# Kernel optimization log

Measured on AMD Instinct MI355X. Metric: run time of the kernel, lower is better.

The kernel has to match this reference:

```python
import jax, jax.numpy as jnp
import numpy as np

N_NODES = 100000
N_EDGES = 1600000
H = 64
N_LAYERS = 3
NUM_APPS = max(1, N_LAYERS - 1)  # forward applies layer once, then while l>1 loop


def setup_inputs() -> dict:
    key = jax.random.key(0)
    k1, k2, k3, k4, k5 = jax.random.split(key, 5)
    features = jax.random.normal(k1, (N_NODES, H), dtype=jnp.float32)
    W = jax.random.normal(k2, (H, H), dtype=jnp.float32) / np.sqrt(H)
    b = jax.random.normal(k3, (H,), dtype=jnp.float32) * 0.01
    src = jax.random.randint(k4, (N_EDGES,), 0, N_NODES, dtype=jnp.int64)
    dst = jax.random.randint(k5, (N_EDGES,), 0, N_NODES, dtype=jnp.int64)
    return {"features": features, "W": W, "b": b, "src": src, "dst": dst}


def reference(features, W, b, src, dst):
    n = features.shape[0]
    ones = jnp.ones(src.shape[0], dtype=features.dtype)
    # DGL GraphConv norm='both': symmetric normalization, degrees clamped >= 1
    deg_out = jax.ops.segment_sum(ones, src, num_segments=n)
    deg_in = jax.ops.segment_sum(ones, dst, num_segments=n)
    inv_sqrt_out = jnp.clip(deg_out, 1.0, None) ** -0.5  # [N]
    inv_sqrt_in = jnp.clip(deg_in, 1.0, None) ** -0.5    # [N]

    h = features
    for _ in range(NUM_APPS):  # shared-weight GraphConv + ReLU, applied n_layers-1 times
        msg = (h * inv_sqrt_out[:, None])[src]                   # [E, H] gather
        agg = jax.ops.segment_sum(msg, dst, num_segments=n)      # [N, H] scatter-add
        h = jax.nn.relu((agg * inv_sqrt_in[:, None]) @ W + b)    # [N, H]
    return h
```

## Files before the change

### kernel.cpp

```cpp
#include <hip/hip_runtime.h>
#include <hip/hip_fp16.h>

#define N_NODES 100000
#define N_EDGES 1600000
#define HDIM 64
#define NPB 512
#define NPB_SHIFT 9
#define NBUCK ((N_NODES + NPB - 1) / NPB)
#define NCHUNK 512
#define CHUNK (N_EDGES / NCHUNK)

__global__ void hist_kernel(const int* __restrict__ src, const int* __restrict__ dst,
                            int* __restrict__ hbD, int* __restrict__ hbS) {
    __shared__ int hD[NBUCK], hS[NBUCK];
    int t = threadIdx.x, blk = blockIdx.x;
    for (int i = t; i < NBUCK; i += 256) { hD[i] = 0; hS[i] = 0; }
    __syncthreads();
    int e0 = blk * CHUNK;
    for (int i = t; i < CHUNK; i += 256) {
        atomicAdd(&hD[dst[e0 + i] >> NPB_SHIFT], 1);
        atomicAdd(&hS[src[e0 + i] >> NPB_SHIFT], 1);
    }
    __syncthreads();
    for (int i = t; i < NBUCK; i += 256) {
        hbD[i * NCHUNK + blk] = hD[i];
        hbS[i * NCHUNK + blk] = hS[i];
    }
}

__global__ void chunk_scan_kernel(const int* __restrict__ hbD, const int* __restrict__ hbS,
                                  int* __restrict__ pbD, int* __restrict__ pbS,
                                  int* __restrict__ totD, int* __restrict__ totS) {
    __shared__ int s[NCHUNK];
    int b = blockIdx.x, t = threadIdx.x;
    int v = hbD[b * NCHUNK + t];
    s[t] = v;
    __syncthreads();
    for (int off = 1; off < NCHUNK; off <<= 1) {
        int x = (t >= off) ? s[t - off] : 0;
        __syncthreads(); s[t] += x; __syncthreads();
    }
    pbD[b * NCHUNK + t] = s[t] - v;
    if (t == NCHUNK - 1) totD[b] = s[t];
    __syncthreads();
    v = hbS[b * NCHUNK + t];
    s[t] = v;
    __syncthreads();
    for (int off = 1; off < NCHUNK; off <<= 1) {
        int x = (t >= off) ? s[t - off] : 0;
        __syncthreads(); s[t] += x; __syncthreads();
    }
    pbS[b * NCHUNK + t] = s[t] - v;
    if (t == NCHUNK - 1) totS[b] = s[t];
}

__global__ void bucket_base_kernel(const int* __restrict__ totD, const int* __restrict__ totS,
                                   int* __restrict__ baseD, int* __restrict__ baseS) {
    __shared__ int s[256];
    int t = threadIdx.x;
    int v = (t < NBUCK) ? totD[t] : 0;
    s[t] = v;
    __syncthreads();
    for (int off = 1; off < 256; off <<= 1) {
        int x = (t >= off) ? s[t - off] : 0;
        __syncthreads(); s[t] += x; __syncthreads();
    }
    if (t < NBUCK) baseD[t] = s[t] - v;
    __syncthreads();
    v = (t < NBUCK) ? totS[t] : 0;
    s[t] = v;
    __syncthreads();
    for (int off = 1; off < 256; off <<= 1) {
        int x = (t >= off) ? s[t - off] : 0;
        __syncthreads(); s[t] += x; __syncthreads();
    }
    if (t < NBUCK) baseS[t] = s[t] - v;
}

__global__ void place_kernel(const int* __restrict__ src, const int* __restrict__ dst,
                             const int* __restrict__ baseD, const int* __restrict__ pbD,
                             const int* __restrict__ baseS, const int* __restrict__ pbS,
                             unsigned int* __restrict__ bufD, unsigned short* __restrict__ bufS) {
    __shared__ int curD[NBUCK], curS[NBUCK];
    int t = threadIdx.x, blk = blockIdx.x;
    for (int i = t; i < NBUCK; i += 256) {
        curD[i] = baseD[i] + pbD[i * NCHUNK + blk];
        curS[i] = baseS[i] + pbS[i * NCHUNK + blk];
    }
    __syncthreads();
    int e0 = blk * CHUNK;
    for (int i = t; i < CHUNK; i += 256) {
        int s = src[e0 + i], d = dst[e0 + i];
        int pd = atomicAdd(&curD[d >> NPB_SHIFT], 1);
        bufD[pd] = (unsigned)s | ((unsigned)(d & (NPB - 1)) << 17);
        int ps = atomicAdd(&curS[s >> NPB_SHIFT], 1);
        bufS[ps] = (unsigned short)(s & (NPB - 1));
    }
}

__global__ void bucket_dst_kernel(const unsigned int* __restrict__ bufD,
                                  const int* __restrict__ baseD, const int* __restrict__ totD,
                                  int* __restrict__ csr_src, int* __restrict__ offsets,
                                  float* __restrict__ inv_in) {
    __shared__ int cnt[NPB], pre[NPB], cur[NPB];
    int b = blockIdx.x, t = threadIdx.x;
    int ebase = baseD[b], ecnt = totD[b];
    cnt[t] = 0;
    __syncthreads();
    for (int i = t; i < ecnt; i += NPB)
        atomicAdd(&cnt[bufD[ebase + i] >> 17], 1);
    __syncthreads();
    int v = cnt[t];
    pre[t] = v;
    __syncthreads();
    for (int off = 1; off < NPB; off <<= 1) {
        int x = (t >= off) ? pre[t - off] : 0;
        __syncthreads(); pre[t] += x; __syncthreads();
    }
    int excl = pre[t] - v;
    cur[t] = excl;
    int node = b * NPB + t;
    if (node < N_NODES) {
        offsets[node] = ebase + excl;
        inv_in[node] = rsqrtf((float)max(v, 1));
    } else if (node == N_NODES) {
        offsets[N_NODES] = N_EDGES;
    }
    __syncthreads();
    for (int i = t; i < ecnt; i += NPB) {
        unsigned int en = bufD[ebase + i];
        int l = (int)(en >> 17);
        int pos = atomicAdd(&cur[l], 1);
        csr_src[ebase + pos] = (int)(en & 0x1FFFFu);
    }
}

__global__ void bucket_src_kernel(const unsigned short* __restrict__ bufS,
                                  const int* __restrict__ baseS, const int* __restrict__ totS,
                                  float* __restrict__ inv_out) {
    __shared__ int cnt[NPB];
    int b = blockIdx.x, t = threadIdx.x;
    int ebase = baseS[b], ecnt = totS[b];
    cnt[t] = 0;
    __syncthreads();
    for (int i = t; i < ecnt; i += NPB)
        atomicAdd(&cnt[(int)bufS[ebase + i]], 1);
    __syncthreads();
    int node = b * NPB + t;
    if (node < N_NODES) inv_out[node] = rsqrtf((float)max(cnt[t], 1));
}

__device__ inline uint2 f4_to_h4(float4 a) {
    __half2 lo = __floats2half2_rn(a.x, a.y);
    __half2 hi = __floats2half2_rn(a.z, a.w);
    uint2 r;
    r.x = *(unsigned*)&lo;
    r.y = *(unsigned*)&hi;
    return r;
}

__global__ void dense_kernel(const float* __restrict__ h, const float* __restrict__ inv_out,
                             const float* __restrict__ W, uint2* __restrict__ hw, int n) {
    __shared__ float Wlds[HDIM * HDIM];
    __shared__ float Alds[32][HDIM + 1];
    int t = threadIdx.x;
    int r0 = blockIdx.x * 32;

    for (int i = t; i < HDIM * HDIM / 4; i += 256)
        ((float4*)Wlds)[i] = ((const float4*)W)[i];

    for (int i = t; i < 512; i += 256) {
        int r = i >> 4;
        int c4 = i & 15;
        int row = r0 + r;
        float4 v = make_float4(0.f, 0.f, 0.f, 0.f);
        float s = 0.f;
        if (row < n) {
            v = ((const float4*)h)[(long long)row * 16 + c4];
            s = inv_out[row];
        }
        Alds[r][c4 * 4 + 0] = v.x * s;
        Alds[r][c4 * 4 + 1] = v.y * s;
        Alds[r][c4 * 4 + 2] = v.z * s;
        Alds[r][c4 * 4 + 3] = v.w * s;
    }
    __syncthreads();

    int tx = t & 15;
    int ty = t >> 4;
    float4 acc0 = make_float4(0.f, 0.f, 0.f, 0.f);
    float4 acc1 = acc0;

#pragma unroll 8
    for (int k = 0; k < HDIM; ++k) {
        float4 w = ((const float4*)(Wlds + k * HDIM))[tx];
        float a0 = Alds[2 * ty + 0][k];
        float a1 = Alds[2 * ty + 1][k];
        acc0.x = fmaf(a0, w.x, acc0.x); acc0.y = fmaf(a0, w.y, acc0.y);
        acc0.z = fmaf(a0, w.z, acc0.z); acc0.w = fmaf(a0, w.w, acc0.w);
        acc1.x = fmaf(a1, w.x, acc1.x); acc1.y = fmaf(a1, w.y, acc1.y);
        acc1.z = fmaf(a1, w.z, acc1.z); acc1.w = fmaf(a1, w.w, acc1.w);
    }

    int rb = r0 + 2 * ty;
    if (rb + 0 < n) hw[(long long)(rb + 0) * 16 + tx] = f4_to_h4(acc0);
    if (rb + 1 < n) hw[(long long)(rb + 1) * 16 + tx] = f4_to_h4(acc1);
}

__global__ void gather_kernel(const uint4* __restrict__ hw, const float* __restrict__ inv_in,
                              const int* __restrict__ offsets, const int* __restrict__ csr_src,
                              const float* __restrict__ bias, float* __restrict__ out, int n) {
    int t = threadIdx.x;
    int wave = t >> 6, lane = t & 63;
    int g = lane >> 3, gl = lane & 7;
    int row = blockIdx.x * 32 + wave * 8 + g;
    if (row >= n) return;

    float acc0 = 0.f, acc1 = 0.f, acc2 = 0.f, acc3 = 0.f;
    float acc4 = 0.f, acc5 = 0.f, acc6 = 0.f, acc7 = 0.f;

    int start = offsets[row];
    int end   = offsets[row + 1];
    int gbase = g << 3;

    int jb = start;
    int mm = end - jb; if (mm > 8) mm = 8;
    int sidx = (mm > 0 && gl < mm) ? csr_src[jb + gl] : 0;

    while (jb < end) {
        int jb2 = jb + 8;
        int mm2 = end - jb2; if (mm2 > 8) mm2 = 8;
        int sidx2 = (jb2 < end && gl < mm2) ? csr_src[jb2 + gl] : 0;

        if (mm == 8) {
#pragma unroll
            for (int j = 0; j < 8; ++j) {
                int s = __shfl(sidx, gbase + j, 64);
                uint4 u = hw[(long long)s * 8 + gl];
                float2 f0 = __half22float2(*(__half2*)&u.x);
                float2 f1 = __half22float2(*(__half2*)&u.y);
                float2 f2 = __half22float2(*(__half2*)&u.z);
                float2 f3 = __half22float2(*(__half2*)&u.w);
                acc0 += f0.x; acc1 += f0.y; acc2 += f1.x; acc3 += f1.y;
                acc4 += f2.x; acc5 += f2.y; acc6 += f3.x; acc7 += f3.y;
            }
        } else {
            for (int j = 0; j < mm; ++j) {
                int s = __shfl(sidx, gbase + j, 64);
                uint4 u = hw[(long long)s * 8 + gl];
                float2 f0 = __half22float2(*(__half2*)&u.x);
                float2 f1 = __half22float2(*(__half2*)&u.y);
                float2 f2 = __half22float2(*(__half2*)&u.z);
                float2 f3 = __half22float2(*(__half2*)&u.w);
                acc0 += f0.x; acc1 += f0.y; acc2 += f1.x; acc3 += f1.y;
                acc4 += f2.x; acc5 += f2.y; acc6 += f3.x; acc7 += f3.y;
            }
        }
        jb = jb2; mm = mm2; sidx = sidx2;
    }

    float sc = inv_in[row];
    float4 b0 = ((const float4*)bias)[gl * 2 + 0];
    float4 b1 = ((const float4*)bias)[gl * 2 + 1];
    float4 r0, r1;
    r0.x = fmaxf(fmaf(acc0, sc, b0.x), 0.f);
    r0.y = fmaxf(fmaf(acc1, sc, b0.y), 0.f);
    r0.z = fmaxf(fmaf(acc2, sc, b0.z), 0.f);
    r0.w = fmaxf(fmaf(acc3, sc, b0.w), 0.f);
    r1.x = fmaxf(fmaf(acc4, sc, b1.x), 0.f);
    r1.y = fmaxf(fmaf(acc5, sc, b1.y), 0.f);
    r1.z = fmaxf(fmaf(acc6, sc, b1.z), 0.f);
    r1.w = fmaxf(fmaf(acc7, sc, b1.w), 0.f);
    ((float4*)out)[(long long)row * 16 + gl * 2 + 0] = r0;
    ((float4*)out)[(long long)row * 16 + gl * 2 + 1] = r1;
}

extern "C" void kernel_launch(void* const* d_in, const int* in_sizes, int n_in,
                              void* d_out, int out_size, void* d_ws, size_t ws_size,
                              hipStream_t stream) {
    const float* features = (const float*)d_in[0];
    const float* W        = (const float*)d_in[1];
    const float* b        = (const float*)d_in[2];
    const int*   src      = (const int*)d_in[3];
    const int*   dst      = (const int*)d_in[4];

    float* out = (float*)d_out;

    float* ws = (float*)d_ws;
    uint2* hw = (uint2*)ws;
    unsigned int*   bufD = (unsigned int*)(ws + (size_t)N_NODES * 32);
    unsigned short* bufS = (unsigned short*)(bufD + N_EDGES);
    float* inv_out = (float*)(bufS + N_EDGES);
    float* inv_in  = inv_out + N_NODES;
    int*   offsets = (int*)(inv_in + N_NODES);
    int*   csr_src = offsets + N_NODES + 1;
    int*   hbD     = csr_src + N_EDGES;
    int*   hbS     = hbD + NBUCK * NCHUNK;
    int*   pbD     = hbS + NBUCK * NCHUNK;
    int*   pbS     = pbD + NBUCK * NCHUNK;
    int*   totD    = pbS + NBUCK * NCHUNK;
    int*   totS    = totD + NBUCK;
    int*   baseD   = totS + NBUCK;
    int*   baseS   = baseD + NBUCK;

    const int N = N_NODES;

    hist_kernel<<<NCHUNK, 256, 0, stream>>>(src, dst, hbD, hbS);
    chunk_scan_kernel<<<NBUCK, NCHUNK, 0, stream>>>(hbD, hbS, pbD, pbS, totD, totS);
    bucket_base_kernel<<<1, 256, 0, stream>>>(totD, totS, baseD, baseS);
    place_kernel<<<NCHUNK, 256, 0, stream>>>(src, dst, baseD, pbD, baseS, pbS, bufD, bufS);
    bucket_dst_kernel<<<NBUCK, NPB, 0, stream>>>(bufD, baseD, totD, csr_src, offsets, inv_in);
    bucket_src_kernel<<<NBUCK, NPB, 0, stream>>>(bufS, baseS, totS, inv_out);

    int dense_blocks  = (N + 31) / 32;
    int gather_blocks = (N + 31) / 32;

    dense_kernel<<<dense_blocks, 256, 0, stream>>>(features, inv_out, W, hw, N);
    gather_kernel<<<gather_blocks, 256, 0, stream>>>((const uint4*)hw, inv_in, offsets, csr_src, b, out, N);

    dense_kernel<<<dense_blocks, 256, 0, stream>>>(out, inv_out, W, hw, N);
    gather_kernel<<<gather_blocks, 256, 0, stream>>>((const uint4*)hw, inv_in, offsets, csr_src, b, out, N);
}
```

Before: 247.6 us.

## Fuse CSR build stages into one persistent kernel with grid barriers

Replaces six separate kernels for the histogram, scans, placement and per-bucket sorting with one 256-block persistent kernel that separates the phases with atomic-counter grid barriers. The point is to remove launch gaps and small serial kernels between phases. Bucket size drops to 256 nodes, which lets the per-source bucket buffer shrink to bytes. The cost is less parallelism in each phase, since only 256 blocks run. It also relies on all blocks being co-resident, and the barrier needs an extra memset launch.

Result: slower. 392.1 us (+58.4%).

```diff
diff --git a/kernel.cpp b/kernel.cpp
--- a/kernel.cpp
+++ b/kernel.cpp
@@ -4,150 +4,158 @@
 #define N_NODES 100000
 #define N_EDGES 1600000
 #define HDIM 64
-#define NPB 512
-#define NPB_SHIFT 9
-#define NBUCK ((N_NODES + NPB - 1) / NPB)
-#define NCHUNK 512
+#define NPB 256
+#define NPB_SHIFT 8
+#define NBUCK 391
+#define GRID_B 256
+#define NCHUNK 256
 #define CHUNK (N_EDGES / NCHUNK)
-
-__global__ void hist_kernel(const int* __restrict__ src, const int* __restrict__ dst,
-                            int* __restrict__ hbD, int* __restrict__ hbS) {
-    __shared__ int hD[NBUCK], hS[NBUCK];
+#define NTASK (2 * NBUCK)
+
+__device__ __forceinline__ void grid_barrier(int* cnt, int id) {
+    __syncthreads();
+    if (threadIdx.x == 0) {
+        __threadfence();
+        __hip_atomic_fetch_add(&cnt[id], 1, __ATOMIC_RELEASE, __HIP_MEMORY_SCOPE_AGENT);
+        while (__hip_atomic_load(&cnt[id], __ATOMIC_ACQUIRE, __HIP_MEMORY_SCOPE_AGENT) < GRID_B)
+            __builtin_amdgcn_s_sleep(1);
+        __threadfence();
+    }
+    __syncthreads();
+}
+
+__global__ void __launch_bounds__(256)
+setup_kernel(const int* __restrict__ src, const int* __restrict__ dst,
+             int* __restrict__ hbD, int* __restrict__ hbS,
+             int* __restrict__ pbD, int* __restrict__ pbS,
+             int* __restrict__ totD, int* __restrict__ totS,
+             int* __restrict__ baseD, int* __restrict__ baseS,
+             unsigned int* __restrict__ bufD, unsigned char* __restrict__ bufS,
+             int* __restrict__ csr_src, int* __restrict__ offsets,
+             float* __restrict__ inv_in, float* __restrict__ inv_out,
+             int* __restrict__ bar) {
+    __shared__ int sm[1024];
     int t = threadIdx.x, blk = blockIdx.x;
-    for (int i = t; i < NBUCK; i += 256) { hD[i] = 0; hS[i] = 0; }
-    __syncthreads();
     int e0 = blk * CHUNK;
-    for (int i = t; i < CHUNK; i += 256) {
-        atomicAdd(&hD[dst[e0 + i] >> NPB_SHIFT], 1);
-        atomicAdd(&hS[src[e0 + i] >> NPB_SHIFT], 1);
-    }
-    __syncthreads();
-    for (int i = t; i < NBUCK; i += 256) {
-        hbD[i * NCHUNK + blk] = hD[i];
-        hbS[i * NCHUNK + blk] = hS[i];
-    }
-}
-
-__global__ void chunk_scan_kernel(const int* __restrict__ hbD, const int* __restrict__ hbS,
-                                  int* __restrict__ pbD, int* __restrict__ pbS,
-                                  int* __restrict__ totD, int* __restrict__ totS) {
-    __shared__ int s[NCHUNK];
-    int b = blockIdx.x, t = threadIdx.x;
-    int v = hbD[b * NCHUNK + t];
-    s[t] = v;
-    __syncthreads();
-    for (int off = 1; off < NCHUNK; off <<= 1) {
-        int x = (t >= off) ? s[t - off] : 0;
-        __syncthreads(); s[t] += x; __syncthreads();
-    }
-    pbD[b * NCHUNK + t] = s[t] - v;
-    if (t == NCHUNK - 1) totD[b] = s[t];
-    __syncthreads();
-    v = hbS[b * NCHUNK + t];
-    s[t] = v;
-    __syncthreads();
-    for (int off = 1; off < NCHUNK; off <<= 1) {
-        int x = (t >= off) ? s[t - off] : 0;
-        __syncthreads(); s[t] += x; __syncthreads();
-    }
-    pbS[b * NCHUNK + t] = s[t] - v;
-    if (t == NCHUNK - 1) totS[b] = s[t];
-}
-
-__global__ void bucket_base_kernel(const int* __restrict__ totD, const int* __restrict__ totS,
-                                   int* __restrict__ baseD, int* __restrict__ baseS) {
-    __shared__ int s[256];
-    int t = threadIdx.x;
-    int v = (t < NBUCK) ? totD[t] : 0;
-    s[t] = v;
-    __syncthreads();
-    for (int off = 1; off < 256; off <<= 1) {
-        int x = (t >= off) ? s[t - off] : 0;
-        __syncthreads(); s[t] += x; __syncthreads();
-    }
-    if (t < NBUCK) baseD[t] = s[t] - v;
-    __syncthreads();
-    v = (t < NBUCK) ? totS[t] : 0;
-    s[t] = v;
-    __syncthreads();
-    for (int off = 1; off < 256; off <<= 1) {
-        int x = (t >= off) ? s[t - off] : 0;
-        __syncthreads(); s[t] += x; __syncthreads();
-    }
-    if (t < NBUCK) baseS[t] = s[t] - v;
-}
-
-__global__ void place_kernel(const int* __restrict__ src, const int* __restrict__ dst,
-                             const int* __restrict__ baseD, const int* __restrict__ pbD,
-                             const int* __restrict__ baseS, const int* __restrict__ pbS,
-                             unsigned int* __restrict__ bufD, unsigned short* __restrict__ bufS) {
-    __shared__ int curD[NBUCK], curS[NBUCK];
-    int t = threadIdx.x, blk = blockIdx.x;
-    for (int i = t; i < NBUCK; i += 256) {
-        curD[i] = baseD[i] + pbD[i * NCHUNK + blk];
-        curS[i] = baseS[i] + pbS[i * NCHUNK + blk];
-    }
-    __syncthreads();
-    int e0 = blk * CHUNK;
-    for (int i = t; i < CHUNK; i += 256) {
-        int s = src[e0 + i], d = dst[e0 + i];
-        int pd = atomicAdd(&curD[d >> NPB_SHIFT], 1);
-        bufD[pd] = (unsigned)s | ((unsigned)(d & (NPB - 1)) << 17);
-        int ps = atomicAdd(&curS[s >> NPB_SHIFT], 1);
-        bufS[ps] = (unsigned short)(s & (NPB - 1));
-    }
-}
-
-__global__ void bucket_dst_kernel(const unsigned int* __restrict__ bufD,
-                                  const int* __restrict__ baseD, const int* __restrict__ totD,
-                                  int* __restrict__ csr_src, int* __restrict__ offsets,
-                                  float* __restrict__ inv_in) {
-    __shared__ int cnt[NPB], pre[NPB], cur[NPB];
-    int b = blockIdx.x, t = threadIdx.x;
-    int ebase = baseD[b], ecnt = totD[b];
-    cnt[t] = 0;
-    __syncthreads();
-    for (int i = t; i < ecnt; i += NPB)
-        atomicAdd(&cnt[bufD[ebase + i] >> 17], 1);
-    __syncthreads();
-    int v = cnt[t];
-    pre[t] = v;
-    __syncthreads();
-    for (int off = 1; off < NPB; off <<= 1) {
-        int x = (t >= off) ? pre[t - off] : 0;
-        __syncthreads(); pre[t] += x; __syncthreads();
-    }
-    int excl = pre[t] - v;
-    cur[t] = excl;
-    int node = b * NPB + t;
-    if (node < N_NODES) {
-        offsets[node] = ebase + excl;
-        inv_in[node] = rsqrtf((float)max(v, 1));
-    } else if (node == N_NODES) {
-        offsets[N_NODES] = N_EDGES;
-    }
-    __syncthreads();
-    for (int i = t; i < ecnt; i += NPB) {
-        unsigned int en = bufD[ebase + i];
-        int l = (int)(en >> 17);
-        int pos = atomicAdd(&cur[l], 1);
-        csr_src[ebase + pos] = (int)(en & 0x1FFFFu);
-    }
-}
-
-__global__ void bucket_src_kernel(const unsigned short* __restrict__ bufS,
-                                  const int* __restrict__ baseS, const int* __restrict__ totS,
-                                  float* __restrict__ inv_out) {
-    __shared__ int cnt[NPB];
-    int b = blockIdx.x, t = threadIdx.x;
-    int ebase = baseS[b], ecnt = totS[b];
-    cnt[t] = 0;
-    __syncthreads();
-    for (int i = t; i < ecnt; i += NPB)
-        atomicAdd(&cnt[(int)bufS[ebase + i]], 1);
-    __syncthreads();
-    int node = b * NPB + t;
-    if (node < N_NODES) inv_out[node] = rsqrtf((float)max(cnt[t], 1));
+
+    {
+        int* hD = sm;
+        int* hS = sm + NBUCK;
+        for (int i = t; i < 2 * NBUCK; i += 256) sm[i] = 0;
+        __syncthreads();
+        for (int i = t; i < CHUNK; i += 256) {
+            atomicAdd(&hD[dst[e0 + i] >> NPB_SHIFT], 1);
+            atomicAdd(&hS[src[e0 + i] >> NPB_SHIFT], 1);
+        }
+        __syncthreads();
+        for (int i = t; i < NBUCK; i += 256) {
+            hbD[i * NCHUNK + blk] = hD[i];
+            hbS[i * NCHUNK + blk] = hS[i];
+        }
+    }
+    grid_barrier(bar, 0);
+
+    for (int task = blk; task < NTASK; task += GRID_B) {
+        const int* h; int* pb; int* tot; int b;
+        if (task < NBUCK) { h = hbD; pb = pbD; tot = totD; b = task; }
+        else              { h = hbS; pb = pbS; tot = totS; b = task - NBUCK; }
+        int v = h[b * NCHUNK + t];
+        sm[t] = v;
+        __syncthreads();
+        for (int off = 1; off < 256; off <<= 1) {
+            int x = (t >= off) ? sm[t - off] : 0;
+            __syncthreads(); sm[t] += x; __syncthreads();
+        }
+        pb[b * NCHUNK + t] = sm[t] - v;
+        if (t == 255) tot[b] = sm[t];
+        __syncthreads();
+    }
+    grid_barrier(bar, 1);
+
+    if (blk < 2) {
+        const int* tot = blk ? totS : totD;
+        int* base = blk ? baseS : baseD;
+        int i0 = 2 * t, i1 = 2 * t + 1;
+        int v0 = (i0 < NBUCK) ? tot[i0] : 0;
+        int v1 = (i1 < NBUCK) ? tot[i1] : 0;
+        int p = v0 + v1;
+        sm[t] = p;
+        __syncthreads();
+        for (int off = 1; off < 256; off <<= 1) {
+            int x = (t >= off) ? sm[t - off] : 0;
+            __syncthreads(); sm[t] += x; __syncthreads();
+        }
+        int ep = sm[t] - p;
+        if (i0 < NBUCK) base[i0] = ep;
+        if (i1 < NBUCK) base[i1] = ep + v0;
+    }
+    grid_barrier(bar, 2);
+
+    {
+        int* curD = sm;
+        int* curS = sm + NBUCK;
+        for (int i = t; i < NBUCK; i += 256) {
+            curD[i] = baseD[i] + pbD[i * NCHUNK + blk];
+            curS[i] = baseS[i] + pbS[i * NCHUNK + blk];
+        }
+        __syncthreads();
+        for (int i = t; i < CHUNK; i += 256) {
+            int s = src[e0 + i], d = dst[e0 + i];
+            int pd = atomicAdd(&curD[d >> NPB_SHIFT], 1);
+            bufD[pd] = (unsigned)s | ((unsigned)(d & (NPB - 1)) << 17);
+            int ps = atomicAdd(&curS[s >> NPB_SHIFT], 1);
+            bufS[ps] = (unsigned char)(s & (NPB - 1));
+        }
+    }
+    grid_barrier(bar, 3);
+
+    {
+        int* cnt = sm;
+        int* pre = sm + 256;
+        int* cur = sm + 512;
+        for (int task = blk; task < NTASK; task += GRID_B) {
+            __syncthreads();
+            if (task < NBUCK) {
+                int b = task, ebase = baseD[b], ecnt = totD[b];
+                cnt[t] = 0;
+                __syncthreads();
+                for (int i = t; i < ecnt; i += 256)
+                    atomicAdd(&cnt[(int)(bufD[ebase + i] >> 17)], 1);
+                __syncthreads();
+                int v = cnt[t];
+                pre[t] = v;
+                __syncthreads();
+                for (int off = 1; off < 256; off <<= 1) {
+                    int x = (t >= off) ? pre[t - off] : 0;
+                    __syncthreads(); pre[t] += x; __syncthreads();
+                }
+                int excl = pre[t] - v;
+                cur[t] = excl;
+                int node = b * NPB + t;
+                if (node < N_NODES) {
+                    offsets[node] = ebase + excl;
+                    inv_in[node] = rsqrtf((float)max(v, 1));
+                } else if (node == N_NODES) {
+                    offsets[N_NODES] = N_EDGES;
+                }
+                __syncthreads();
+                for (int i = t; i < ecnt; i += 256) {
+                    unsigned en = bufD[ebase + i];
+                    int pos = atomicAdd(&cur[(int)(en >> 17)], 1);
+                    csr_src[ebase + pos] = (int)(en & 0x1FFFFu);
+                }
+            } else {
+                int b = task - NBUCK, ebase = baseS[b], ecnt = totS[b];
+                cnt[t] = 0;
+                __syncthreads();
+                for (int i = t; i < ecnt; i += 256)
+                    atomicAdd(&cnt[(int)bufS[ebase + i]], 1);
+                __syncthreads();
+                int node = b * NPB + t;
+                if (node < N_NODES) inv_out[node] = rsqrtf((float)max(cnt[t], 1));
+            }
+        }
+    }
 }
 
 __device__ inline uint2 f4_to_h4(float4 a) {
@@ -288,8 +296,8 @@
 
     float* ws = (float*)d_ws;
     uint2* hw = (uint2*)ws;
-    unsigned int*   bufD = (unsigned int*)(ws + (size_t)N_NODES * 32);
-    unsigned short* bufS = (unsigned short*)(bufD + N_EDGES);
+    unsigned int*  bufD = (unsigned int*)(ws + (size_t)N_NODES * 32);
+    unsigned char* bufS = (unsigned char*)(bufD + N_EDGES);
     float* inv_out = (float*)(bufS + N_EDGES);
     float* inv_in  = inv_out + N_NODES;
     int*   offsets = (int*)(inv_in + N_NODES);
@@ -302,15 +310,14 @@
     int*   totS    = totD + NBUCK;
     int*   baseD   = totS + NBUCK;
     int*   baseS   = baseD + NBUCK;
+    int*   bar     = baseS + NBUCK + 16;
 
     const int N = N_NODES;
 
-    hist_kernel<<<NCHUNK, 256, 0, stream>>>(src, dst, hbD, hbS);
-    chunk_scan_kernel<<<NBUCK, NCHUNK, 0, stream>>>(hbD, hbS, pbD, pbS, totD, totS);
-    bucket_base_kernel<<<1, 256, 0, stream>>>(totD, totS, baseD, baseS);
-    place_kernel<<<NCHUNK, 256, 0, stream>>>(src, dst, baseD, pbD, baseS, pbS, bufD, bufS);
-    bucket_dst_kernel<<<NBUCK, NPB, 0, stream>>>(bufD, baseD, totD, csr_src, offsets, inv_in);
-    bucket_src_kernel<<<NBUCK, NPB, 0, stream>>>(bufS, baseS, totS, inv_out);
+    hipMemsetAsync(bar, 0, 16 * sizeof(int), stream);
+    setup_kernel<<<GRID_B, 256, 0, stream>>>(src, dst, hbD, hbS, pbD, pbS, totD, totS,
+                                             baseD, baseS, bufD, bufS, csr_src, offsets,
+                                             inv_in, inv_out, bar);
 
     int dense_blocks  = (N + 31) / 32;
     int gather_blocks = (N + 31) / 32;
```
